# Kernel tuning notes

Measured on AMD Instinct MI355X. Metric: run time of the kernel, lower is better.

The kernel has to match this reference:

```python
import jax, jax.numpy as jnp
import numpy as np

H_DIM = 1152
N_HEADS = 12
HEAD_DIM = H_DIM // N_HEADS  # 96, divisible by 3
SCALE_ROT = 32 // 16  # character_pixel_size // patch_size


def setup_inputs() -> dict:
    key = jax.random.key(0)
    ks = jax.random.split(key, 9)
    std = 1.0 / np.sqrt(H_DIM)
    return {
        "hidden_states": jax.random.normal(ks[0], (8, 1025, H_DIM), dtype=jnp.float32),
        "Wq": jax.random.normal(ks[1], (H_DIM, H_DIM), dtype=jnp.float32) * std,
        "bq": jax.random.normal(ks[2], (H_DIM,), dtype=jnp.float32) * 0.02,
        "Wk": jax.random.normal(ks[3], (H_DIM, H_DIM), dtype=jnp.float32) * std,
        "bk": jax.random.normal(ks[4], (H_DIM,), dtype=jnp.float32) * 0.02,
        "Wv": jax.random.normal(ks[5], (H_DIM, H_DIM), dtype=jnp.float32) * std,
        "bv": jax.random.normal(ks[6], (H_DIM,), dtype=jnp.float32) * 0.02,
        "Wo": jax.random.normal(ks[7], (H_DIM, H_DIM), dtype=jnp.float32) * std,
        "bo": jax.random.normal(ks[8], (H_DIM,), dtype=jnp.float32) * 0.02,
        "rows": 32,
        "cols": 32,
    }


def _rotary_tables(seq_len, rows, cols, dtype):
    # (seq_len, n_triplets) trig tables based on 2-D patch grid position
    inv_freq = 1.0 / (10000.0 ** (jnp.arange(0, HEAD_DIM, 3, dtype=dtype) / (HEAD_DIM * SCALE_ROT)))
    ids = jnp.arange(seq_len)
    cls_offset = 1 if seq_len != rows * cols else 0
    grid_ids = jnp.clip(ids - cls_offset, 0)
    row_ids = (grid_ids // cols).astype(dtype)
    col_ids = (grid_ids % cols).astype(dtype)
    theta = row_ids[:, None] * inv_freq
    psi = col_ids[:, None] * inv_freq
    return jnp.cos(theta), jnp.sin(theta), jnp.cos(psi), jnp.sin(psi)


def _apply_rotary_3d(x, ct, st, cp, sp):
    # x: (b, s, h, d) -> view as (b, s, h, t, 3)
    b, s, h, d = x.shape
    x = x.reshape(b, s, h, d // 3, 3)
    ct = ct[None, :, None, :]
    st = st[None, :, None, :]
    cp = cp[None, :, None, :]
    sp = sp[None, :, None, :]
    x0, x1, x2 = x[..., 0], x[..., 1], x[..., 2]
    r0 = cp * x0 + sp * st * x1 + sp * ct * x2
    r1 = ct * x1 - st * x2
    r2 = -sp * x0 + cp * st * x1 + cp * ct * x2
    return jnp.stack((r0, r1, r2), axis=-1).reshape(b, s, h, d)


def reference(hidden_states, Wq, bq, Wk, bk, Wv, bv, Wo, bo, rows, cols):
    b, s, _ = hidden_states.shape
    dtype = hidden_states.dtype
    scale = HEAD_DIM ** -0.5

    q = (hidden_states @ Wq + bq).reshape(b, s, N_HEADS, HEAD_DIM)
    k = (hidden_states @ Wk + bk).reshape(b, s, N_HEADS, HEAD_DIM)
    v = (hidden_states @ Wv + bv).reshape(b, s, N_HEADS, HEAD_DIM)

    ct, st, cp, sp = _rotary_tables(s, rows, cols, dtype)
    q = _apply_rotary_3d(q, ct, st, cp, sp)
    k = _apply_rotary_3d(k, ct, st, cp, sp)

    # (b, h, s, s) attention scores
    scores = jnp.einsum("bqhd,bkhd->bhqk", q, k) * scale
    probs = jax.nn.softmax(scores.astype(jnp.float32), axis=-1).astype(dtype)
    ctx = jnp.einsum("bhqk,bkhd->bqhd", probs, v).reshape(b, s, H_DIM)
    out = ctx @ Wo + bo
    return out
```

## Files before the change

### kernel.cpp

```cpp
#include <hip/hip_runtime.h>
#include <stdint.h>

#define BATCH 8
#define SEQ   1025
#define HDIM  1152
#define NH    12
#define DH    96
#define MROWS (BATCH*SEQ)
#define N_QKV (3*HDIM)
#define KD    HDIM

typedef __attribute__((ext_vector_type(8))) short short8;
typedef __attribute__((ext_vector_type(4))) short short4_;
typedef __attribute__((ext_vector_type(4))) float float4_;
typedef __attribute__((ext_vector_type(16))) float f32x16;

__device__ inline float bf2f(short s) {
  union { unsigned u; float f; } x; x.u = ((unsigned)(unsigned short)s) << 16; return x.f;
}
__device__ inline short f2bf(float f) {
  union { float f; unsigned u; } x; x.f = f;
  unsigned r = (x.u + 0x7fffu + ((x.u >> 16) & 1u)) >> 16;
  return (short)r;
}

__global__ __launch_bounds__(256) void convx(const float* __restrict__ hs, short* __restrict__ X) {
  int i = blockIdx.x * 256 + threadIdx.x;
  float4_ v = ((const float4_*)hs)[i];
  short4_ o;
  o[0] = f2bf(v[0]); o[1] = f2bf(v[1]); o[2] = f2bf(v[2]); o[3] = f2bf(v[3]);
  ((short4_*)X)[i] = o;
}

__global__ __launch_bounds__(256) void convw_qkv(const float* __restrict__ Wq,
                                                 const float* __restrict__ Wk,
                                                 const float* __restrict__ Wv,
                                                 short* __restrict__ Wt) {
  long e = (long)blockIdx.x * 256 + threadIdx.x;
  int n = (int)(e / KD), k = (int)(e % KD);
  const float* W = n < HDIM ? Wq : (n < 2 * HDIM ? Wk : Wv);
  int nn = n < HDIM ? n : (n < 2 * HDIM ? n - HDIM : n - 2 * HDIM);
  Wt[e] = f2bf(W[(long)k * HDIM + nn]);
}

__global__ __launch_bounds__(256) void convw_o(const float* __restrict__ Wo, short* __restrict__ Wot) {
  long e = (long)blockIdx.x * 256 + threadIdx.x;
  int n = (int)(e / HDIM), k = (int)(e % HDIM);
  Wot[e] = f2bf(Wo[(long)k * HDIM + n]);
}

template<int OUTF32>
__global__ __launch_bounds__(256, 2) void gemm_kernel(
    const short* __restrict__ A, const short* __restrict__ Bt,
    const float* __restrict__ b0, const float* __restrict__ b1, const float* __restrict__ b2,
    void* __restrict__ Cout, const int N) {
  __shared__ short As[4096];
  __shared__ short Bs[4096];
  const int tid = threadIdx.x;
  const int l = tid & 63, w = tid >> 6;
  const int lrow = l & 15, lg = l >> 4;
  const int n0 = blockIdx.x * 128, m0 = blockIdx.y * 128;
  const int wm = (w >> 1) * 64, wn = (w & 1) * 64;

  float4_ acc[4][4];
#pragma unroll
  for (int i = 0; i < 4; ++i)
#pragma unroll
    for (int j = 0; j < 4; ++j) acc[i][j] = (float4_)(0.f);

  const int sr = tid >> 2;
  const int sk = (tid & 3) * 8;
  int ra0 = m0 + sr;       if (ra0 > MROWS - 1) ra0 = MROWS - 1;
  int ra1 = m0 + 64 + sr;  if (ra1 > MROWS - 1) ra1 = MROWS - 1;
  const short* pa0 = A + (long)ra0 * KD + sk;
  const short* pa1 = A + (long)ra1 * KD + sk;
  const short* pb0 = Bt + (long)(n0 + sr) * KD + sk;
  const short* pb1 = Bt + (long)(n0 + 64 + sr) * KD + sk;
  short* la0 = &As[w * 512];
  short* la1 = &As[2048 + w * 512];
  short* lb0 = &Bs[w * 512];
  short* lb1 = &Bs[2048 + w * 512];

  for (int kt = 0; kt < KD / 32; ++kt) {
    __syncthreads();
    const int ko = kt * 32;
    __builtin_amdgcn_global_load_lds((const __attribute__((address_space(1))) void*)(pa0 + ko),
                                     (__attribute__((address_space(3))) void*)la0, 16, 0, 0);
    __builtin_amdgcn_global_load_lds((const __attribute__((address_space(1))) void*)(pa1 + ko),
                                     (__attribute__((address_space(3))) void*)la1, 16, 0, 0);
    __builtin_amdgcn_global_load_lds((const __attribute__((address_space(1))) void*)(pb0 + ko),
                                     (__attribute__((address_space(3))) void*)lb0, 16, 0, 0);
    __builtin_amdgcn_global_load_lds((const __attribute__((address_space(1))) void*)(pb1 + ko),
                                     (__attribute__((address_space(3))) void*)lb1, 16, 0, 0);
    __syncthreads();
    short8 af[4], bf[4];
#pragma unroll
    for (int i = 0; i < 4; ++i) af[i] = *(const short8*)&As[(wm + i * 16 + lrow) * 32 + lg * 8];
#pragma unroll
    for (int j = 0; j < 4; ++j) bf[j] = *(const short8*)&Bs[(wn + j * 16 + lrow) * 32 + lg * 8];
#pragma unroll
    for (int i = 0; i < 4; ++i)
#pragma unroll
      for (int j = 0; j < 4; ++j)
        acc[i][j] = __builtin_amdgcn_mfma_f32_16x16x32_bf16(af[i], bf[j], acc[i][j], 0, 0, 0);
  }

#pragma unroll
  for (int i = 0; i < 4; ++i) {
#pragma unroll
    for (int r = 0; r < 4; ++r) {
      int m = m0 + wm + i * 16 + lg * 4 + r;
      if (m >= MROWS) continue;
#pragma unroll
      for (int j = 0; j < 4; ++j) {
        int n = n0 + wn + j * 16 + lrow;
        float bias = (N == HDIM) ? b0[n]
                                 : (n < HDIM ? b0[n] : (n < 2 * HDIM ? b1[n - HDIM] : b2[n - 2 * HDIM]));
        float v = acc[i][j][r] + bias;
        if (OUTF32) ((float*)Cout)[(long)m * N + n] = v;
        else        ((short*)Cout)[(long)m * N + n] = f2bf(v);
      }
    }
  }
}

__global__ __launch_bounds__(256) void rotary_kernel(short* __restrict__ QKV,
                                                     const int* __restrict__ rowsp,
                                                     const int* __restrict__ colsp) {
  int idx = blockIdx.x * 256 + threadIdx.x;
  int j = idx & 31;
  int t = idx >> 5;
  int h = t % NH;
  int m = t / NH;
  int s = m % SEQ;
  int cols = colsp[0];
  int rws = rowsp[0];
  int off = (SEQ != rws * cols) ? 1 : 0;
  int gid = s - off; if (gid < 0) gid = 0;
  int row = gid / cols, col = gid % cols;
  float invf = exp2f((float)(3 * j) * (-13.287712379549449f / 192.0f));
  float th = row * invf, ps = col * invf;
  float st, ct, sp, cp;
  __sincosf(th, &st, &ct);
  __sincosf(ps, &sp, &cp);
  short* qp = QKV + (long)m * N_QKV + h * DH + 3 * j;
#pragma unroll
  for (int qk = 0; qk < 2; ++qk) {
    short* p = qp + qk * HDIM;
    float x0 = bf2f(p[0]), x1 = bf2f(p[1]), x2 = bf2f(p[2]);
    float r0 =  cp * x0 + sp * st * x1 + sp * ct * x2;
    float r1 =  ct * x1 - st * x2;
    float r2 = -sp * x0 + cp * st * x1 + cp * ct * x2;
    p[0] = f2bf(r0); p[1] = f2bf(r1); p[2] = f2bf(r2);
  }
}

__global__ __launch_bounds__(256) void fragpack(const short* __restrict__ QKV,
                                                short* __restrict__ Kf,
                                                short* __restrict__ Vf) {
  __shared__ short L[64 * 96];
  const int t = blockIdx.x, bh = blockIdx.y;
  const int b = bh / NH, h = bh % NH;
  const int tid = threadIdx.x;
#pragma unroll
  for (int i = 0; i < 3; ++i) {
    int cc = i * 256 + tid;
    int kv = cc / 384;
    int rm = cc % 384;
    int r = rm / 12, m = rm % 12;
    int s = t * 32 + r; if (s > SEQ - 1) s = SEQ - 1;
    const short* src = QKV + (long)(b * SEQ + s) * N_QKV + (kv ? 2 * HDIM : HDIM) + h * DH + m * 8;
    *(short8*)&L[cc * 8] = *(const short8*)src;
  }
  __syncthreads();
#pragma unroll
  for (int i = 0; i < 3; ++i) {
    int oc = i * 256 + tid;
    if (oc < 384) {
      int c = oc / 64, l = oc & 63;
      int qi = l & 31, hi = l >> 5;
      short8 v = *(const short8*)&L[qi * 96 + c * 16 + hi * 8];
      *(short8*)(Kf + (((long)(bh * 33 + t) * 6 + c) * 64 + l) * 8) = v;
    } else {
      int oc2 = oc - 384;
      int d = oc2 / 128, sl = (oc2 / 64) & 1, l = oc2 & 63;
      int qi = l & 31, hi = l >> 5;
      short8 v;
#pragma unroll
      for (int j = 0; j < 8; ++j)
        v[j] = L[32 * 96 + (sl * 16 + hi * 8 + j) * 96 + d * 32 + qi];
      *(short8*)(Vf + ((((long)(bh * 33 + t) * 3 + d) * 2 + sl) * 64 + l) * 8) = v;
    }
  }
}

__global__ __launch_bounds__(128, 3) void attn_kernel(const short* __restrict__ QKV,
                                                      const short* __restrict__ Kf,
                                                      const short* __restrict__ Vf,
                                                      short* __restrict__ CTX) {
  const int tid = threadIdx.x;
  const int l = tid & 63, w = tid >> 6;
  const int qi = l & 31, hi = l >> 5;
  const int bid = blockIdx.x;
  const int xcd = bid & 7, jj = bid >> 3;
  const int bh = xcd * 12 + jj / 17;
  const int qb = jj % 17;
  const int b = bh / NH, h = bh % NH;
  const int s = qb * 64 + w * 32 + qi;
  const int sq = s > SEQ - 1 ? SEQ - 1 : s;

  const float scale = 0.1020620726159658f;
  const short* Qr = QKV + (long)(b * SEQ + sq) * N_QKV + h * DH;
  short8 qf[6];
#pragma unroll
  for (int c = 0; c < 6; ++c) {
    short8 v = *(const short8*)(Qr + c * 16 + hi * 8);
#pragma unroll
    for (int j = 0; j < 8; ++j) v[j] = f2bf(bf2f(v[j]) * scale);
    qf[c] = v;
  }

  const short* Kb = Kf + (long)bh * 33 * 6 * 64 * 8;
  const short* Vb = Vf + (long)bh * 33 * 6 * 64 * 8;

  f32x16 ctxv[3];
#pragma unroll
  for (int d = 0; d < 3; ++d) ctxv[d] = (f32x16)(0.f);
  float m_ = -1e30f, l_ = 0.f;

  for (int t = 0; t < 33; ++t) {
    f32x16 S = (f32x16)(0.f);
#pragma unroll
    for (int c = 0; c < 6; ++c) {
      short8 kf = *(const short8*)(Kb + (((long)t * 6 + c) * 64 + l) * 8);
      S = __builtin_amdgcn_mfma_f32_32x32x16_bf16(kf, qf[c], S, 0, 0, 0);
    }
    if (t == 32) {
      S[0] = hi ? -1e30f : S[0];
#pragma unroll
      for (int r = 1; r < 16; ++r) S[r] = -1e30f;
    }
    float tm = S[0];
#pragma unroll
    for (int r = 1; r < 16; ++r) tm = fmaxf(tm, S[r]);
    tm = fmaxf(tm, __shfl_xor(tm, 32));
    if (!__all(tm - m_ <= 8.f)) {
      float mn = fmaxf(m_, tm);
      float alpha = __expf(m_ - mn);
      m_ = mn;
      l_ *= alpha;
#pragma unroll
      for (int d = 0; d < 3; ++d)
#pragma unroll
        for (int r = 0; r < 16; ++r) ctxv[d][r] *= alpha;
    }
    float ts = 0.f;
#pragma unroll
    for (int r = 0; r < 16; ++r) { float p = __expf(S[r] - m_); S[r] = p; ts += p; }
    ts += __shfl_xor(ts, 32);
    l_ += ts;

    unsigned pk_[8];
#pragma unroll
    for (int j = 0; j < 8; ++j)
      pk_[j] = (unsigned)(unsigned short)f2bf(S[2 * j]) |
               ((unsigned)(unsigned short)f2bf(S[2 * j + 1]) << 16);
    unsigned s0 = hi ? pk_[0] : pk_[2];
    unsigned s1 = hi ? pk_[1] : pk_[3];
    unsigned s2 = hi ? pk_[4] : pk_[6];
    unsigned s3 = hi ? pk_[5] : pk_[7];
    unsigned r0 = __shfl_xor(s0, 32);
    unsigned r1 = __shfl_xor(s1, 32);
    unsigned r2 = __shfl_xor(s2, 32);
    unsigned r3 = __shfl_xor(s3, 32);
    union PF { unsigned u[4]; short8 s8; } f0, f1;
    f0.u[0] = hi ? r0 : pk_[0];
    f0.u[1] = hi ? r1 : pk_[1];
    f0.u[2] = hi ? pk_[2] : r0;
    f0.u[3] = hi ? pk_[3] : r1;
    f1.u[0] = hi ? r2 : pk_[4];
    f1.u[1] = hi ? r3 : pk_[5];
    f1.u[2] = hi ? pk_[6] : r2;
    f1.u[3] = hi ? pk_[7] : r3;

#pragma unroll
    for (int d = 0; d < 3; ++d) {
      const short* Vr = Vb + (((long)t * 3 + d) * 2 * 64) * 8;
      short8 vf0 = *(const short8*)(Vr + l * 8);
      ctxv[d] = __builtin_amdgcn_mfma_f32_32x32x16_bf16(vf0, f0.s8, ctxv[d], 0, 0, 0);
      short8 vf1 = *(const short8*)(Vr + (64 + l) * 8);
      ctxv[d] = __builtin_amdgcn_mfma_f32_32x32x16_bf16(vf1, f1.s8, ctxv[d], 0, 0, 0);
    }
  }

  float invl = 1.f / l_;
  if (s <= SEQ - 1) {
    short* Cr = CTX + (long)(b * SEQ + s) * HDIM + h * DH;
#pragma unroll
    for (int d = 0; d < 3; ++d)
#pragma unroll
      for (int g = 0; g < 4; ++g) {
        short4_ o;
#pragma unroll
        for (int r = 0; r < 4; ++r) o[r] = f2bf(ctxv[d][4 * g + r] * invl);
        *(short4_*)(Cr + d * 32 + 8 * g + 4 * hi) = o;
      }
  }
}

extern "C" void kernel_launch(void* const* d_in, const int* in_sizes, int n_in,
                              void* d_out, int out_size, void* d_ws, size_t ws_size,
                              hipStream_t stream) {
  const float* hs = (const float*)d_in[0];
  const float* Wq = (const float*)d_in[1];
  const float* bq = (const float*)d_in[2];
  const float* Wk = (const float*)d_in[3];
  const float* bk = (const float*)d_in[4];
  const float* Wv = (const float*)d_in[5];
  const float* bv = (const float*)d_in[6];
  const float* Wo = (const float*)d_in[7];
  const float* bo = (const float*)d_in[8];
  const int* rows = (const int*)d_in[9];
  const int* cols = (const int*)d_in[10];
  float* out = (float*)d_out;

  char* ws = (char*)d_ws;
  short* X   = (short*)(ws);
  short* Wt  = (short*)(ws + 18892800);
  short* Wot = (short*)(ws + 26855424);
  short* QKV = (short*)(ws + 29509632);
  short* Vf  = (short*)(ws + 86188032);
  short* CTX = (short*)(ws + 105652224);
  short* Kf  = (short*)(ws);

  convx<<<9225, 256, 0, stream>>>(hs, X);
  convw_qkv<<<15552, 256, 0, stream>>>(Wq, Wk, Wv, Wt);
  convw_o<<<5184, 256, 0, stream>>>(Wo, Wot);
  gemm_kernel<0><<<dim3(27, 65), 256, 0, stream>>>(X, Wt, bq, bk, bv, QKV, N_QKV);
  rotary_kernel<<<12300, 256, 0, stream>>>(QKV, rows, cols);
  fragpack<<<dim3(33, 96), 256, 0, stream>>>(QKV, Kf, Vf);
  attn_kernel<<<1632, 128, 0, stream>>>(QKV, Kf, Vf, CTX);
  gemm_kernel<1><<<dim3(9, 65), 256, 0, stream>>>(CTX, Wot, bo, bo, bo, out, HDIM);
}
```

Measured before the change: 304.3 us.

## Replace 128x128 GEMM with double-buffered 256x256 tile GEMM using 32x32 MFMA

Both projection GEMMs move from 128x128 tiles with 256 threads to 256x256 tiles with 512 threads. The new kernel uses 32x32x16 bf16 MFMA, an XOR-swizzled LDS layout to avoid bank conflicts, and double-buffered global-to-LDS loads with explicit vmcnt waits and barriers. It also raises wave priority around the MFMA blocks and remaps block IDs so consecutive tiles land on the same XCD. The aim is more data reuse per tile and overlap of loads with compute. The cost is fewer workgroups (462 and 165), so the output GEMM may under-fill the GPU, plus one workgroup per CU and heavier register use.

```diff
diff --git a/kernel.cpp b/kernel.cpp
--- a/kernel.cpp
+++ b/kernel.cpp
@@ -9,11 +9,16 @@
 #define MROWS (BATCH*SEQ)
 #define N_QKV (3*HDIM)
 #define KD    HDIM
+#define NTK   36
 
 typedef __attribute__((ext_vector_type(8))) short short8;
 typedef __attribute__((ext_vector_type(4))) short short4_;
 typedef __attribute__((ext_vector_type(4))) float float4_;
 typedef __attribute__((ext_vector_type(16))) float f32x16;
+
+#define AS1 __attribute__((address_space(1)))
+#define AS3 __attribute__((address_space(3)))
+#define BARM() do { asm volatile("" ::: "memory"); __builtin_amdgcn_s_barrier(); asm volatile("" ::: "memory"); } while (0)
 
 __device__ inline float bf2f(short s) {
   union { unsigned u; float f; } x; x.u = ((unsigned)(unsigned short)s) << 16; return x.f;
@@ -50,78 +55,131 @@
 }
 
 template<int OUTF32>
-__global__ __launch_bounds__(256, 2) void gemm_kernel(
+__global__ __launch_bounds__(512, 1) void gemm256(
     const short* __restrict__ A, const short* __restrict__ Bt,
     const float* __restrict__ b0, const float* __restrict__ b1, const float* __restrict__ b2,
-    void* __restrict__ Cout, const int N) {
-  __shared__ short As[4096];
-  __shared__ short Bs[4096];
+    void* __restrict__ Cout, const int N, const int MT) {
+  __shared__ alignas(16) short Lds[32768];
   const int tid = threadIdx.x;
   const int l = tid & 63, w = tid >> 6;
-  const int lrow = l & 15, lg = l >> 4;
-  const int n0 = blockIdx.x * 128, m0 = blockIdx.y * 128;
-  const int wm = (w >> 1) * 64, wn = (w & 1) * 64;
-
-  float4_ acc[4][4];
-#pragma unroll
-  for (int i = 0; i < 4; ++i)
-#pragma unroll
-    for (int j = 0; j < 4; ++j) acc[i][j] = (float4_)(0.f);
-
-  const int sr = tid >> 2;
-  const int sk = (tid & 3) * 8;
-  int ra0 = m0 + sr;       if (ra0 > MROWS - 1) ra0 = MROWS - 1;
-  int ra1 = m0 + 64 + sr;  if (ra1 > MROWS - 1) ra1 = MROWS - 1;
-  const short* pa0 = A + (long)ra0 * KD + sk;
-  const short* pa1 = A + (long)ra1 * KD + sk;
-  const short* pb0 = Bt + (long)(n0 + sr) * KD + sk;
-  const short* pb1 = Bt + (long)(n0 + 64 + sr) * KD + sk;
-  short* la0 = &As[w * 512];
-  short* la1 = &As[2048 + w * 512];
-  short* lb0 = &Bs[w * 512];
-  short* lb1 = &Bs[2048 + w * 512];
-
-  for (int kt = 0; kt < KD / 32; ++kt) {
-    __syncthreads();
-    const int ko = kt * 32;
-    __builtin_amdgcn_global_load_lds((const __attribute__((address_space(1))) void*)(pa0 + ko),
-                                     (__attribute__((address_space(3))) void*)la0, 16, 0, 0);
-    __builtin_amdgcn_global_load_lds((const __attribute__((address_space(1))) void*)(pa1 + ko),
-                                     (__attribute__((address_space(3))) void*)la1, 16, 0, 0);
-    __builtin_amdgcn_global_load_lds((const __attribute__((address_space(1))) void*)(pb0 + ko),
-                                     (__attribute__((address_space(3))) void*)lb0, 16, 0, 0);
-    __builtin_amdgcn_global_load_lds((const __attribute__((address_space(1))) void*)(pb1 + ko),
-                                     (__attribute__((address_space(3))) void*)lb1, 16, 0, 0);
-    __syncthreads();
-    short8 af[4], bf[4];
-#pragma unroll
-    for (int i = 0; i < 4; ++i) af[i] = *(const short8*)&As[(wm + i * 16 + lrow) * 32 + lg * 8];
-#pragma unroll
-    for (int j = 0; j < 4; ++j) bf[j] = *(const short8*)&Bs[(wn + j * 16 + lrow) * 32 + lg * 8];
-#pragma unroll
-    for (int i = 0; i < 4; ++i)
-#pragma unroll
-      for (int j = 0; j < 4; ++j)
-        acc[i][j] = __builtin_amdgcn_mfma_f32_16x16x32_bf16(af[i], bf[j], acc[i][j], 0, 0, 0);
-  }
-
-#pragma unroll
-  for (int i = 0; i < 4; ++i) {
-#pragma unroll
-    for (int r = 0; r < 4; ++r) {
-      int m = m0 + wm + i * 16 + lg * 4 + r;
-      if (m >= MROWS) continue;
-#pragma unroll
-      for (int j = 0; j < 4; ++j) {
-        int n = n0 + wn + j * 16 + lrow;
-        float bias = (N == HDIM) ? b0[n]
-                                 : (n < HDIM ? b0[n] : (n < 2 * HDIM ? b1[n - HDIM] : b2[n - 2 * HDIM]));
-        float v = acc[i][j][r] + bias;
-        if (OUTF32) ((float*)Cout)[(long)m * N + n] = v;
-        else        ((short*)Cout)[(long)m * N + n] = f2bf(v);
+  const int col = l & 31, hi = l >> 5;
+  const int wr = w >> 2, wc = w & 3;
+
+  const int nwg = gridDim.x;
+  const int qq = nwg >> 3, r8 = nwg & 7;
+  const int xcd = blockIdx.x & 7, loc = blockIdx.x >> 3;
+  const int wg = (xcd < r8 ? xcd * (qq + 1) : r8 * (qq + 1) + (xcd - r8) * qq) + loc;
+  const int mt = wg % MT, nt = wg / MT;
+  const int m0 = mt * 256, n0 = nt * 256;
+
+  const int key = (tid >> 3) & 7;
+  const short* asrc[2]; const short* bsrc[2];
+#pragma unroll
+  for (int i = 0; i < 2; ++i) {
+    int g = (i * 512 + tid) ^ key;
+    int rowl = g >> 2, colE = (g & 3) * 8;
+    int ra = m0 + rowl; if (ra > MROWS - 1) ra = MROWS - 1;
+    int rb = n0 + rowl; if (rb > N - 1) rb = N - 1;
+    asrc[i] = A + (long)ra * KD + colE;
+    bsrc[i] = Bt + (long)rb * KD + colE;
+  }
+
+#define STAGE_A(buf, kt_, i) \
+  __builtin_amdgcn_global_load_lds((const AS1 void*)(asrc[i] + (kt_) * 32), \
+      (AS3 void*)(&Lds[(buf) * 8192 + (i) * 4096 + tid * 8]), 16, 0, 0)
+#define STAGE_B(buf, kt_, i) \
+  __builtin_amdgcn_global_load_lds((const AS1 void*)(bsrc[i] + (kt_) * 32), \
+      (AS3 void*)(&Lds[16384 + (buf) * 8192 + (i) * 4096 + tid * 8]), 16, 0, 0)
+
+  const int keyx = ((col >> 1) & 7) << 3;
+  const int fcol = hi * 8;
+#define LDSA(buf, mi, ks) (*(const short8*)&Lds[(buf) * 8192 + \
+    ((((wr * 128 + (mi) * 32 + col) << 5) + ((ks) << 4) + fcol) ^ keyx)])
+#define LDSB(buf, nj, ks) (*(const short8*)&Lds[16384 + (buf) * 8192 + \
+    ((((wc * 64 + (nj) * 32 + col) << 5) + ((ks) << 4) + fcol) ^ keyx)])
+#define MFMA32(a, b, c) __builtin_amdgcn_mfma_f32_32x32x16_bf16(a, b, c, 0, 0, 0)
+
+  f32x16 acc[4][2];
+#pragma unroll
+  for (int mi = 0; mi < 4; ++mi)
+#pragma unroll
+    for (int nj = 0; nj < 2; ++nj) acc[mi][nj] = (f32x16)(0.f);
+
+  STAGE_A(0, 0, 0); STAGE_A(0, 0, 1);
+  STAGE_B(0, 0, 0); STAGE_B(0, 0, 1);
+  STAGE_B(1, 1, 0); STAGE_B(1, 1, 1);
+  asm volatile("s_waitcnt vmcnt(2)" ::: "memory");
+  BARM();
+
+  for (int kt = 0; kt < NTK; ++kt) {
+    const int cur = kt & 1, nxt = cur ^ 1;
+    short8 b00 = LDSB(cur, 0, 0), b01 = LDSB(cur, 0, 1);
+    short8 b10 = LDSB(cur, 1, 0), b11 = LDSB(cur, 1, 1);
+    short8 a00 = LDSA(cur, 0, 0), a01 = LDSA(cur, 0, 1);
+    short8 a10 = LDSA(cur, 1, 0), a11 = LDSA(cur, 1, 1);
+    if (kt + 1 < NTK) { STAGE_A(nxt, kt + 1, 0); STAGE_A(nxt, kt + 1, 1); }
+    BARM();
+    __builtin_amdgcn_s_setprio(1);
+    acc[0][0] = MFMA32(a00, b00, acc[0][0]);
+    acc[0][1] = MFMA32(a00, b10, acc[0][1]);
+    acc[1][0] = MFMA32(a10, b00, acc[1][0]);
+    acc[1][1] = MFMA32(a10, b10, acc[1][1]);
+    acc[0][0] = MFMA32(a01, b01, acc[0][0]);
+    acc[0][1] = MFMA32(a01, b11, acc[0][1]);
+    acc[1][0] = MFMA32(a11, b01, acc[1][0]);
+    acc[1][1] = MFMA32(a11, b11, acc[1][1]);
+    __builtin_amdgcn_s_setprio(0);
+    BARM();
+    short8 a20 = LDSA(cur, 2, 0), a21 = LDSA(cur, 2, 1);
+    short8 a30 = LDSA(cur, 3, 0), a31 = LDSA(cur, 3, 1);
+    if (kt + 2 < NTK) { STAGE_B(cur, kt + 2, 0); STAGE_B(cur, kt + 2, 1); }
+    if (kt < NTK - 2) asm volatile("s_waitcnt vmcnt(2)" ::: "memory");
+    else              asm volatile("s_waitcnt vmcnt(0)" ::: "memory");
+    BARM();
+    __builtin_amdgcn_s_setprio(1);
+    acc[2][0] = MFMA32(a20, b00, acc[2][0]);
+    acc[2][1] = MFMA32(a20, b10, acc[2][1]);
+    acc[3][0] = MFMA32(a30, b00, acc[3][0]);
+    acc[3][1] = MFMA32(a30, b10, acc[3][1]);
+    acc[2][0] = MFMA32(a21, b01, acc[2][0]);
+    acc[2][1] = MFMA32(a21, b11, acc[2][1]);
+    acc[3][0] = MFMA32(a31, b01, acc[3][0]);
+    acc[3][1] = MFMA32(a31, b11, acc[3][1]);
+    __builtin_amdgcn_s_setprio(0);
+    BARM();
+  }
+
+  float bias[2];
+#pragma unroll
+  for (int nj = 0; nj < 2; ++nj) {
+    int cn = n0 + wc * 64 + nj * 32 + col;
+    float bv_ = 0.f;
+    if (cn < N) bv_ = (N == HDIM) ? b0[cn]
+                                  : (cn < HDIM ? b0[cn] : (cn < 2 * HDIM ? b1[cn - HDIM] : b2[cn - 2 * HDIM]));
+    bias[nj] = bv_;
+  }
+#pragma unroll
+  for (int mi = 0; mi < 4; ++mi)
+#pragma unroll
+    for (int g = 0; g < 4; ++g)
+#pragma unroll
+      for (int t2 = 0; t2 < 4; ++t2) {
+        int rowi = m0 + wr * 128 + mi * 32 + g * 8 + hi * 4 + t2;
+        if (rowi >= MROWS) continue;
+#pragma unroll
+        for (int nj = 0; nj < 2; ++nj) {
+          int cn = n0 + wc * 64 + nj * 32 + col;
+          if (cn >= N) continue;
+          float v = acc[mi][nj][g * 4 + t2] + bias[nj];
+          if (OUTF32) ((float*)Cout)[(long)rowi * N + cn] = v;
+          else        ((short*)Cout)[(long)rowi * N + cn] = f2bf(v);
+        }
       }
-    }
-  }
+#undef STAGE_A
+#undef STAGE_B
+#undef LDSA
+#undef LDSB
+#undef MFMA32
 }
 
 __global__ __launch_bounds__(256) void rotary_kernel(short* __restrict__ QKV,
@@ -177,19 +235,19 @@
   for (int i = 0; i < 3; ++i) {
     int oc = i * 256 + tid;
     if (oc < 384) {
-      int c = oc / 64, l = oc & 63;
-      int qi = l & 31, hi = l >> 5;
+      int c = oc / 64, ll = oc & 63;
+      int qi = ll & 31, hi = ll >> 5;
       short8 v = *(const short8*)&L[qi * 96 + c * 16 + hi * 8];
-      *(short8*)(Kf + (((long)(bh * 33 + t) * 6 + c) * 64 + l) * 8) = v;
+      *(short8*)(Kf + (((long)(bh * 33 + t) * 6 + c) * 64 + ll) * 8) = v;
     } else {
       int oc2 = oc - 384;
-      int d = oc2 / 128, sl = (oc2 / 64) & 1, l = oc2 & 63;
-      int qi = l & 31, hi = l >> 5;
+      int d = oc2 / 128, sl = (oc2 / 64) & 1, ll = oc2 & 63;
+      int qi = ll & 31, hi = ll >> 5;
       short8 v;
 #pragma unroll
       for (int j = 0; j < 8; ++j)
         v[j] = L[32 * 96 + (sl * 16 + hi * 8 + j) * 96 + d * 32 + qi];
-      *(short8*)(Vf + ((((long)(bh * 33 + t) * 3 + d) * 2 + sl) * 64 + l) * 8) = v;
+      *(short8*)(Vf + ((((long)(bh * 33 + t) * 3 + d) * 2 + sl) * 64 + ll) * 8) = v;
     }
   }
 }
@@ -336,9 +394,9 @@
   convx<<<9225, 256, 0, stream>>>(hs, X);
   convw_qkv<<<15552, 256, 0, stream>>>(Wq, Wk, Wv, Wt);
   convw_o<<<5184, 256, 0, stream>>>(Wo, Wot);
-  gemm_kernel<0><<<dim3(27, 65), 256, 0, stream>>>(X, Wt, bq, bk, bv, QKV, N_QKV);
+  gemm256<0><<<462, 512, 0, stream>>>(X, Wt, bq, bk, bv, QKV, N_QKV, 33);
   rotary_kernel<<<12300, 256, 0, stream>>>(QKV, rows, cols);
   fragpack<<<dim3(33, 96), 256, 0, stream>>>(QKV, Kf, Vf);
   attn_kernel<<<1632, 128, 0, stream>>>(QKV, Kf, Vf, CTX);
-  gemm_kernel<1><<<dim3(9, 65), 256, 0, stream>>>(CTX, Wot, bo, bo, bo, out, HDIM);
-}
+  gemm256<1><<<165, 512, 0, stream>>>(CTX, Wot, bo, bo, bo, out, HDIM, 33);
+}
```

Result: slower. 317.5 us (+4.3%).
